# Performance work log

Measured on AMD Instinct MI355X. Metric: run time of the kernel, lower is better.

Reference implementation:

```python
import jax, jax.numpy as jnp
import numpy as np
from functools import partial

DIM = 192
HEADS = 8
DN = ('NCHW', 'OIHW', 'NCHW')


def conv1x1(x, w):
    # w: [O, I, 1, 1]
    return jax.lax.conv_general_dilated(x, w, (1, 1), 'VALID', dimension_numbers=DN)


def dwconv3x3(x, w):
    # w: [C, 1, 3, 3], depthwise
    return jax.lax.conv_general_dilated(x, w, (1, 1), 'SAME', dimension_numbers=DN,
                                        feature_group_count=x.shape[1])


def l2norm(x, eps=1e-12):
    n = jnp.sqrt(jnp.sum(x * x, axis=-1, keepdims=True))
    return x / jnp.maximum(n, eps)


def compute_attention(q, k_s, v_s, k_c, v_c, temperature, beta):
    b, c, h, w = q.shape
    hw = h * w
    r = lambda t: t.reshape(b, HEADS, c // HEADS, hw)  # b head c (h w)
    qn = l2norm(r(q))
    ks = l2norm(r(k_s))
    kc = l2norm(r(k_c))
    vs, vc = r(v_s), r(v_c)
    # channel-wise attention: [b, head, c, c]
    sa = jax.nn.softmax(jnp.einsum('bhcn,bhdn->bhcd', qn, ks) * temperature, axis=-1)
    so = jnp.einsum('bhcd,bhdn->bhcn', sa, vs)
    ca = jax.nn.softmax(-(jnp.einsum('bhcn,bhdn->bhcd', qn, kc) * temperature), axis=-1)
    co = jnp.einsum('bhcd,bhdn->bhcn', ca, vc)
    out = jax.nn.sigmoid(beta) * so + co
    return out.reshape(b, c, h, w)


def setup_inputs() -> dict:
    key = jax.random.key(0)
    ks = jax.random.split(key, 8)
    B, C, H, W = 8, DIM, 128, 128
    s = 0.02
    return {
        'x1': jax.random.normal(ks[0], (B, C, H, W), jnp.float32),
        'x2': jax.random.normal(ks[1], (B, C, H, W), jnp.float32),
        'w_qkv1': jax.random.normal(ks[2], (3 * C, C, 1, 1), jnp.float32) * s,
        'w_dw1': jax.random.normal(ks[3], (3 * C, 1, 3, 3), jnp.float32) * s,
        'w_qkv2': jax.random.normal(ks[4], (3 * C, C, 1, 1), jnp.float32) * s,
        'w_dw2': jax.random.normal(ks[5], (3 * C, 1, 3, 3), jnp.float32) * s,
        'w_proj': jax.random.normal(ks[6], (C, C, 1, 1), jnp.float32) * s,
        'temperature': jnp.ones((HEADS, 1, 1), jnp.float32),
        'beta': jnp.zeros((1,), jnp.float32),
    }


def reference(x1, x2, w_qkv1, w_dw1, w_qkv2, w_dw2, w_proj, temperature, beta):
    qkv1 = dwconv3x3(conv1x1(x1, w_qkv1), w_dw1)
    q1, k1, v1 = jnp.split(qkv1, 3, axis=1)
    qkv2 = dwconv3x3(conv1x1(x2, w_qkv2), w_dw2)
    q2, k2, v2 = jnp.split(qkv2, 3, axis=1)
    e1 = compute_attention(q1, k1, v1, k2, v2, temperature, beta)
    e2 = compute_attention(q2, k2, v2, k1, v1, temperature, beta)
    return conv1x1(e1, w_proj), conv1x1(e2, w_proj)
```

## Files before the change

kernel.cpp:

```cpp
#include <hip/hip_runtime.h>

typedef unsigned short u16;
typedef unsigned int u32;

#define NB 8
#define NCH 192
#define NC3 576
#define NHW 16384
#define NHEADS 8

typedef __attribute__((ext_vector_type(8))) short s16x8;
typedef __attribute__((ext_vector_type(4))) float f32x4;

__device__ __forceinline__ float bf2f(u32 h) {
  return __uint_as_float(h << 16);
}
__device__ __forceinline__ u16 f2bf(float f) {
  u32 u = __float_as_uint(f);
  u = (u + 0x7fffu + ((u >> 16) & 1u)) >> 16;
  return (u16)u;
}
__device__ __forceinline__ u32 pk2(u16 a, u16 b) { return (u32)a | ((u32)b << 16); }

__device__ __forceinline__ int swz(int row) { return ((row >> 1) & 7) << 4; }

__device__ __forceinline__ void gl_lds16(const void* g, void* s) {
  __builtin_amdgcn_global_load_lds((const __attribute__((address_space(1))) unsigned int*)g,
                                   (__attribute__((address_space(3))) unsigned int*)s, 16, 0, 0);
}

__global__ __launch_bounds__(256) void wcast_kernel(
    const float* __restrict__ w1, const float* __restrict__ w2,
    u16* __restrict__ o1, u16* __restrict__ o2, float* __restrict__ norms2,
    float* __restrict__ G) {
  int i = blockIdx.x * 256 + threadIdx.x;
  if (i < NC3 * NCH) {
    o1[i] = f2bf(w1[i]);
    o2[i] = f2bf(w2[i]);
  }
  if (i < 4 * NB * NCH) norms2[i] = 0.f;
  if (i < NB * NHEADS * 2304) G[i] = 0.f;
}

__device__ __forceinline__ void conv_b_load(const float* __restrict__ x, int b, int nbase,
                                            int kb, int w, int l, float2 (&val)[16]) {
  const float* xr = x + (((size_t)(b * NCH + kb + w * 16)) << 14) + nbase + l * 2;
#pragma unroll
  for (int jj = 0; jj < 16; ++jj)
    val[jj] = *(const float2*)(xr + ((size_t)jj << 14));
}

__device__ __forceinline__ void conv_b_write(char* smem, int w, int l,
                                             const float2 (&val)[16]) {
#pragma unroll
  for (int nn = 0; nn < 2; ++nn) {
    const int row = l * 2 + nn;
    u32 p[8];
#pragma unroll
    for (int q = 0; q < 8; ++q) {
      const float a = nn ? val[2 * q].y : val[2 * q].x;
      const float bb = nn ? val[2 * q + 1].y : val[2 * q + 1].x;
      p[q] = pk2(f2bf(a), f2bf(bb));
    }
    char* base = smem + 49152 + row * 128;
    *(uint4*)(base + ((w * 32 + 0) ^ swz(row))) = make_uint4(p[0], p[1], p[2], p[3]);
    *(uint4*)(base + ((w * 32 + 16) ^ swz(row))) = make_uint4(p[4], p[5], p[6], p[7]);
  }
}

__device__ __forceinline__ void conv_a_glds(char* smem, const u16* __restrict__ wbf,
                                            int obase, int kb, int w, int l, int buf) {
#pragma unroll
  for (int i = 0; i < 6; ++i) {
    const int grp = i * 4 + w;
    const int row = grp * 8 + (l >> 3);
    const int cb = ((l & 7) * 16) ^ swz(row);
    const char* src = (const char*)wbf + (size_t)(obase + row) * 384 + kb * 2 + cb;
    gl_lds16(src, smem + buf * 24576 + grp * 1024);
  }
}

__global__ __launch_bounds__(256) void conv_mfma_kernel(
    const float* __restrict__ x1, const u16* __restrict__ wbf1, u16* __restrict__ pre1,
    const float* __restrict__ x2, const u16* __restrict__ wbf2, u16* __restrict__ pre2) {
  __shared__ char smem[65536];
  const int bid = blockIdx.x;
  const int id = (bid & 7) * 768 + (bid >> 3);
  const int mod = (id >= 3072) ? 1 : 0;
  const int idm = id - mod * 3072;
  const float* x = mod ? x2 : x1;
  const u16* wbf = mod ? wbf2 : wbf1;
  u16* pre = mod ? pre2 : pre1;
  const int b = idm / 384;
  const int rr = idm % 384;
  const int nbase = (rr / 3) * 128;
  const int obase = (rr % 3) * 192;
  const int tid = threadIdx.x;
  const int w = tid >> 6, l = tid & 63;
  const int wr = w >> 1, wc = w & 1;

  f32x4 acc[6][4];
#pragma unroll
  for (int m = 0; m < 6; ++m)
#pragma unroll
    for (int nf = 0; nf < 4; ++nf) acc[m][nf] = (f32x4)0.f;

  float2 fB[16];
  conv_b_load(x, b, nbase, 0, w, l, fB);
  conv_a_glds(smem, wbf, obase, 0, w, l, 0);
  conv_b_write(smem, w, l, fB);
  __syncthreads();

  for (int t = 0; t < 3; ++t) {
    const int cur = t & 1;
    const int nxt = cur ^ 1;
    if (t < 2) {
      conv_b_load(x, b, nbase, (t + 1) * 64, w, l, fB);
      conv_a_glds(smem, wbf, obase, (t + 1) * 64, w, l, nxt);
    }
#pragma unroll
    for (int kk = 0; kk < 2; ++kk) {
      s16x8 a[6], bv[4];
      const int cbk = kk * 64 + (l >> 4) * 16;
#pragma unroll
      for (int m = 0; m < 6; ++m) {
        const int rowA = wr * 96 + m * 16 + (l & 15);
        a[m] = *(const s16x8*)(smem + cur * 24576 + rowA * 128 + (cbk ^ swz(rowA)));
      }
#pragma unroll
      for (int nf = 0; nf < 4; ++nf) {
        const int rowB = wc * 64 + nf * 16 + (l & 15);
        bv[nf] = *(const s16x8*)(smem + 49152 + rowB * 128 + (cbk ^ swz(rowB)));
      }
#pragma unroll
      for (int m = 0; m < 6; ++m)
#pragma unroll
        for (int nf = 0; nf < 4; ++nf)
          acc[m][nf] = __builtin_amdgcn_mfma_f32_16x16x32_bf16(a[m], bv[nf], acc[m][nf], 0, 0, 0);
    }
    __syncthreads();
    if (t < 2) {
      conv_b_write(smem, w, l, fB);
      __syncthreads();
    }
  }
  u16* cw = (u16*)(smem) + w * 16 * 72;
#pragma unroll
  for (int m = 0; m < 6; ++m) {
#pragma unroll
    for (int nf = 0; nf < 4; ++nf)
#pragma unroll
      for (int r = 0; r < 4; ++r)
        cw[((l >> 4) * 4 + r) * 72 + nf * 16 + (l & 15)] = f2bf(acc[m][nf][r]);
#pragma unroll
    for (int p = 0; p < 2; ++p) {
      const int chunk = p * 64 + l;
      const int row = chunk >> 3, cg = chunk & 7;
      uint4 v = *(const uint4*)(cw + row * 72 + cg * 8);
      const int o = obase + wr * 96 + m * 16 + row;
      const int n = nbase + wc * 64 + cg * 8;
      *(uint4*)(pre + (((size_t)b * NC3 + o) << 14) + n) = v;
    }
  }
}

__device__ __forceinline__ void dw_body(float* red, const u16* __restrict__ in,
                                        const float* __restrict__ wdw, u16* __restrict__ out,
                                        float* __restrict__ norms2, const int mod,
                                        const size_t t, const int tid) {
  const int l = tid & 63;
  const int xc = (int)(t & 15);
  const int yy = (int)((t >> 4) & 127);
  const int bc = (int)(t >> 11);
  const int c = bc % NC3;
  const int b = bc / NC3;
  const u16* p = in + ((size_t)bc << 14);
  const float* wc = wdw + c * 9;
  const int x0 = xc * 8;

  float a[3][10];
#pragma unroll
  for (int r = 0; r < 3; ++r) {
    const int y2 = yy + r - 1;
    if ((unsigned)y2 < 128u) {
      const u16* row = p + (y2 << 7);
      uint4 v = *(const uint4*)(row + x0);
      a[r][1] = bf2f(v.x & 0xffff); a[r][2] = bf2f(v.x >> 16);
      a[r][3] = bf2f(v.y & 0xffff); a[r][4] = bf2f(v.y >> 16);
      a[r][5] = bf2f(v.z & 0xffff); a[r][6] = bf2f(v.z >> 16);
      a[r][7] = bf2f(v.w & 0xffff); a[r][8] = bf2f(v.w >> 16);
    } else {
#pragma unroll
      for (int j = 1; j < 9; ++j) a[r][j] = 0.f;
    }
    const float lf = __shfl(a[r][8], (l - 1) & 63, 64);
    const float rt = __shfl(a[r][1], (l + 1) & 63, 64);
    a[r][0] = (xc > 0) ? lf : 0.f;
    a[r][9] = (xc < 15) ? rt : 0.f;
  }
  const float w00 = wc[0], w01 = wc[1], w02 = wc[2];
  const float w10 = wc[3], w11 = wc[4], w12 = wc[5];
  const float w20 = wc[6], w21 = wc[7], w22 = wc[8];
  u16 o[8];
  float ssq = 0.f;
#pragma unroll
  for (int j = 0; j < 8; ++j) {
    float s = a[0][j] * w00;
    s = fmaf(a[0][j + 1], w01, s);
    s = fmaf(a[0][j + 2], w02, s);
    s = fmaf(a[1][j], w10, s);
    s = fmaf(a[1][j + 1], w11, s);
    s = fmaf(a[1][j + 2], w12, s);
    s = fmaf(a[2][j], w20, s);
    s = fmaf(a[2][j + 1], w21, s);
    s = fmaf(a[2][j + 2], w22, s);
    ssq = fmaf(s, s, ssq);
    o[j] = f2bf(s);
  }
  *(uint4*)(out + (t << 3)) =
      make_uint4(pk2(o[0], o[1]), pk2(o[2], o[3]), pk2(o[4], o[5]), pk2(o[6], o[7]));

  if (c < 384) {
#pragma unroll
    for (int off = 32; off > 0; off >>= 1) ssq += __shfl_down(ssq, off, 64);
    if ((tid & 63) == 0) red[tid >> 6] = ssq;
    __syncthreads();
    if (tid == 0) {
      const int tt = (c < 192) ? mod : 2 + mod;
      atomicAdd(&norms2[(tt * NB + b) * NCH + (c % NCH)], red[0] + red[1] + red[2] + red[3]);
    }
  }
}

__global__ __launch_bounds__(256) void dwconv_kernel(
    const u16* __restrict__ in, const float* __restrict__ wdw, u16* __restrict__ out,
    float* __restrict__ norms2, const int mod) {
  __shared__ float red[4];
  dw_body(red, in, wdw, out, norms2, mod,
          (size_t)blockIdx.x * 256 + threadIdx.x, threadIdx.x);
}

__global__ __launch_bounds__(256) void dwm_kernel(
    const u16* __restrict__ pre1, const float* __restrict__ wdw1, u16* __restrict__ qkv1,
    const u16* __restrict__ pre2, const float* __restrict__ wdw2, u16* __restrict__ qkv2,
    float* __restrict__ norms2) {
  __shared__ float red[4];
  const size_t t = (size_t)blockIdx.x * 256 + threadIdx.x;
  const int bc = (int)(t >> 11);
  const int mod = (bc >= NB * NC3) ? 1 : 0;
  const size_t tm = t - ((size_t)mod * NB * NC3 << 11);
  if (mod)
    dw_body(red, pre2, wdw2, qkv2, norms2, 1, tm, threadIdx.x);
  else
    dw_body(red, pre1, wdw1, qkv1, norms2, 0, tm, threadIdx.x);
}

__global__ __launch_bounds__(256) void gram_mfma_kernel(
    const u16* __restrict__ qkv1, const u16* __restrict__ qkv2, float* __restrict__ G) {
  const int nc = blockIdx.x, h = blockIdx.y, b = blockIdx.z;
  const int tid = threadIdx.x;
  const int w = tid >> 6, l = tid & 63;

  const u16* qp[3];
  const u16* kp[3];
#pragma unroll
  for (int m = 0; m < 3; ++m) {
    const int rq = m * 16 + (l & 15);
    const int cc = h * 24 + (rq < 24 ? rq : rq - 24);
    const u16* basep = (rq < 24) ? qkv1 : qkv2;
    qp[m] = basep + (((size_t)b * NC3 + cc) << 14);
    kp[m] = basep + (((size_t)b * NC3 + 192 + cc) << 14);
  }
  const int kbase = nc * 1024 + w * 256 + (l >> 4) * 8;

  f32x4 acc[3][3];
#pragma unroll
  for (int m = 0; m < 3; ++m)
#pragma unroll
    for (int nf = 0; nf < 3; ++nf) acc[m][nf] = (f32x4)0.f;

  for (int t = 0; t < 8; ++t) {
    const int ko = kbase + t * 32;
    s16x8 a[3], bv[3];
#pragma unroll
    for (int m = 0; m < 3; ++m) {
      a[m] = *(const s16x8*)(qp[m] + ko);
      bv[m] = *(const s16x8*)(kp[m] + ko);
    }
#pragma unroll
    for (int m = 0; m < 3; ++m)
#pragma unroll
      for (int nf = 0; nf < 3; ++nf)
        acc[m][nf] = __builtin_amdgcn_mfma_f32_16x16x32_bf16(a[m], bv[nf], acc[m][nf], 0, 0, 0);
  }

  __shared__ float red[4][48][48];
#pragma unroll
  for (int m = 0; m < 3; ++m)
#pragma unroll
    for (int nf = 0; nf < 3; ++nf)
#pragma unroll
      for (int r = 0; r < 4; ++r)
        red[w][m * 16 + (l >> 4) * 4 + r][nf * 16 + (l & 15)] = acc[m][nf][r];
  __syncthreads();
  float* dst = G + ((size_t)b * 8 + h) * 2304;
  for (int e = tid; e < 2304; e += 256) {
    const int rr = e / 48, cc = e % 48;
    atomicAdd(&dst[e], red[0][rr][cc] + red[1][rr][cc] + red[2][rr][cc] + red[3][rr][cc]);
  }
}

__global__ __launch_bounds__(256) void softmax_wcat_kernel(
    const float* __restrict__ G, const float* __restrict__ norms2,
    const float* __restrict__ temperature, const float* __restrict__ beta,
    const float* __restrict__ wproj, u16* __restrict__ Wcat) {
  const int bh = blockIdx.x;
  const int b = bh >> 3, h = bh & 7;
  __shared__ float sm[4][24][24];
  __shared__ float nrm[4][24];
  const int tid = threadIdx.x;
  if (tid < 96) {
    int t = tid / 24, ci = tid % 24;
    nrm[t][ci] = fmaxf(sqrtf(norms2[(t * NB + b) * NCH + h * 24 + ci]), 1e-12f);
  }
  __syncthreads();
  const float T = temperature[h];
  const float sigB = 1.f / (1.f + expf(-beta[0]));
  if (tid < 96) {
    const int m = tid / 24, r = tid % 24;
    const float* Gb = G + (size_t)bh * 2304;
    const int gr = (m >= 2) ? 24 + r : r;
    const int gc0 = (m == 1 || m == 2) ? 24 : 0;
    const float* qn = (m >= 2) ? nrm[1] : nrm[0];
    const float* kn = (m == 1 || m == 2) ? nrm[3] : nrm[2];
    const float sign = (m == 0 || m == 2) ? 1.f : -1.f;
    const float qs = sign * T / qn[r];
    float L[24], mx = -1e30f;
#pragma unroll
    for (int cc = 0; cc < 24; ++cc) {
      L[cc] = Gb[gr * 48 + gc0 + cc] * qs / kn[cc];
      mx = fmaxf(mx, L[cc]);
    }
    float ssum = 0.f;
#pragma unroll
    for (int cc = 0; cc < 24; ++cc) {
      L[cc] = expf(L[cc] - mx);
      ssum += L[cc];
    }
    const float inv = 1.f / ssum;
#pragma unroll
    for (int cc = 0; cc < 24; ++cc) sm[m][r][cc] = L[cc] * inv;
  }
  __syncthreads();
  for (int e = tid; e < 384 * 48; e += 256) {
    const int o = e / 48, dc = e % 48;
    const int part = dc / 24, d = dc % 24;
    const int oc = (o < 192) ? o : o - 192;
    int m;
    float scale;
    if (o < 192) { m = part ? 1 : 0; scale = part ? 1.f : sigB; }
    else         { m = part ? 2 : 3; scale = part ? sigB : 1.f; }
    float s = 0.f;
#pragma unroll
    for (int ci = 0; ci < 24; ++ci) s += wproj[oc * 192 + h * 24 + ci] * sm[m][ci][d];
    Wcat[((size_t)b * 384 + o) * 384 + part * 192 + h * 24 + d] = f2bf(s * scale);
  }
}

__device__ __forceinline__ void fin_b_load(const u16* __restrict__ qkv1,
                                           const u16* __restrict__ qkv2,
                                           int b, int nbase, int kb, int w, int l,
                                           u32 (&val)[16]) {
  const u16* vbase = (kb < 192) ? qkv1 + (((size_t)b * NC3 + 384 + kb) << 14)
                                : qkv2 + (((size_t)b * NC3 + 384 + kb - 192) << 14);
  const u16* p0 = vbase + (((size_t)(w * 16)) << 14) + nbase + l * 2;
#pragma unroll
  for (int jj = 0; jj < 16; ++jj)
    val[jj] = *(const u32*)(p0 + ((size_t)jj << 14));
}

__device__ __forceinline__ void fin_b_write(char* smem, int w, int l,
                                            const u32 (&val)[16]) {
#pragma unroll
  for (int nn = 0; nn < 2; ++nn) {
    const int row = l * 2 + nn;
    u32 p[8];
#pragma unroll
    for (int q = 0; q < 8; ++q) {
      const u32 a = (val[2 * q] >> (nn * 16)) & 0xffffu;
      const u32 bb = (val[2 * q + 1] >> (nn * 16)) & 0xffffu;
      p[q] = a | (bb << 16);
    }
    char* base = smem + 32768 + row * 128;
    *(uint4*)(base + ((w * 32 + 0) ^ swz(row))) = make_uint4(p[0], p[1], p[2], p[3]);
    *(uint4*)(base + ((w * 32 + 16) ^ swz(row))) = make_uint4(p[4], p[5], p[6], p[7]);
  }
}

__device__ __forceinline__ void fin_a_glds(char* smem, const u16* __restrict__ Wcat,
                                           int b, int obase, int kb, int w, int l, int buf) {
#pragma unroll
  for (int i = 0; i < 4; ++i) {
    const int grp = i * 4 + w;
    const int row = grp * 8 + (l >> 3);
    const int cb = ((l & 7) * 16) ^ swz(row);
    const char* src = (const char*)Wcat + ((size_t)b * 384 + obase + row) * 768 + kb * 2 + cb;
    gl_lds16(src, smem + buf * 16384 + grp * 1024);
  }
}

__global__ __launch_bounds__(256) void final_mfma_kernel(
    const u16* __restrict__ qkv1, const u16* __restrict__ qkv2,
    const u16* __restrict__ Wcat, float* __restrict__ out) {
  __shared__ char smem[49152];
  const int bid = blockIdx.x;
  const int id = (bid & 7) * 384 + (bid >> 3);
  const int b = id / 384;
  const int rr2 = id % 384;
  const int nbase = (rr2 / 3) * 128;
  const int obase = (rr2 % 3) * 128;
  const int tid = threadIdx.x;
  const int w = tid >> 6, l = tid & 63;
  const int wr = w >> 1, wc = w & 1;

  f32x4 acc[4][4];
#pragma unroll
  for (int m = 0; m < 4; ++m)
#pragma unroll
    for (int nf = 0; nf < 4; ++nf) acc[m][nf] = (f32x4)0.f;

  u32 fV[16];
  fin_b_load(qkv1, qkv2, b, nbase, 0, w, l, fV);
  fin_a_glds(smem, Wcat, b, obase, 0, w, l, 0);
  fin_b_write(smem, w, l, fV);
  __syncthreads();

  for (int t = 0; t < 6; ++t) {
    const int cur = t & 1;
    const int nxt = cur ^ 1;
    if (t < 5) {
      fin_b_load(qkv1, qkv2, b, nbase, (t + 1) * 64, w, l, fV);
      fin_a_glds(smem, Wcat, b, obase, (t + 1) * 64, w, l, nxt);
    }
#pragma unroll
    for (int kk = 0; kk < 2; ++kk) {
      s16x8 a[4], bv[4];
      const int cbk = kk * 64 + (l >> 4) * 16;
#pragma unroll
      for (int m = 0; m < 4; ++m) {
        const int rowA = wr * 64 + m * 16 + (l & 15);
        a[m] = *(const s16x8*)(smem + cur * 16384 + rowA * 128 + (cbk ^ swz(rowA)));
      }
#pragma unroll
      for (int nf = 0; nf < 4; ++nf) {
        const int rowB = wc * 64 + nf * 16 + (l & 15);
        bv[nf] = *(const s16x8*)(smem + 32768 + rowB * 128 + (cbk ^ swz(rowB)));
      }
#pragma unroll
      for (int m = 0; m < 4; ++m)
#pragma unroll
        for (int nf = 0; nf < 4; ++nf)
          acc[m][nf] = __builtin_amdgcn_mfma_f32_16x16x32_bf16(a[m], bv[nf], acc[m][nf], 0, 0, 0);
    }
    __syncthreads();
    if (t < 5) {
      fin_b_write(smem, w, l, fV);
      __syncthreads();
    }
  }
  float* cw = (float*)(smem + w * 4352);
#pragma unroll
  for (int m = 0; m < 4; ++m) {
#pragma unroll
    for (int nf = 0; nf < 4; ++nf)
#pragma unroll
      for (int r = 0; r < 4; ++r)
        cw[((l >> 4) * 4 + r) * 68 + nf * 16 + (l & 15)] = acc[m][nf][r];
#pragma unroll
    for (int p = 0; p < 4; ++p) {
      const int chunk = p * 64 + l;
      const int row = chunk >> 4, cg = chunk & 15;
      f32x4 v = *(const f32x4*)(cw + row * 68 + cg * 4);
      const int o = obase + wr * 64 + m * 16 + row;
      const int n = nbase + wc * 64 + cg * 4;
      float* dst = (o < 192) ? out + (((size_t)b * NCH + o) << 14) + n
                             : out + 25165824 + (((size_t)b * NCH + o - 192) << 14) + n;
      __builtin_nontemporal_store(v, (f32x4*)dst);
    }
  }
}

extern "C" void kernel_launch(void* const* d_in, const int* in_sizes, int n_in,
                              void* d_out, int out_size, void* d_ws, size_t ws_size,
                              hipStream_t stream) {
  (void)in_sizes; (void)n_in; (void)out_size;
  const float* x1 = (const float*)d_in[0];
  const float* x2 = (const float*)d_in[1];
  const float* w_qkv1 = (const float*)d_in[2];
  const float* w_dw1 = (const float*)d_in[3];
  const float* w_qkv2 = (const float*)d_in[4];
  const float* w_dw2 = (const float*)d_in[5];
  const float* w_proj = (const float*)d_in[6];
  const float* temperature = (const float*)d_in[7];
  const float* beta = (const float*)d_in[8];
  float* out = (float*)d_out;

  char* wsb = (char*)d_ws;
  const size_t BUF = 150994944;
  const bool big = ws_size >= 607395840;

  u16* pre1 = (u16*)(wsb);
  u16* qkv1 = (u16*)(wsb + BUF);
  u16* pre2 = (u16*)(wsb + 2 * BUF);
  u16* qkv2 = big ? (u16*)(wsb + 3 * BUF) : pre1;
  char* tail = big ? (wsb + 4 * BUF) : (wsb + 3 * BUF);
  u16* wbf1 = (u16*)(tail);
  u16* wbf2 = (u16*)(tail + 221184);
  float* norms2 = (float*)(tail + 442368);
  float* G = (float*)(tail + 466944);
  u16* WcatBf = (u16*)(tail + 1056768);

  const int dwblocks = (int)(((size_t)NB * NC3 * NHW) / (256 * 8));

  wcast_kernel<<<576, 256, 0, stream>>>(w_qkv1, w_qkv2, wbf1, wbf2, norms2, G);
  conv_mfma_kernel<<<6144, 256, 0, stream>>>(x1, wbf1, pre1, x2, wbf2, pre2);
  if (big) {
    dwm_kernel<<<2 * dwblocks, 256, 0, stream>>>(pre1, w_dw1, qkv1, pre2, w_dw2, qkv2, norms2);
  } else {
    dwconv_kernel<<<dwblocks, 256, 0, stream>>>(pre1, w_dw1, qkv1, norms2, 0);
    dwconv_kernel<<<dwblocks, 256, 0, stream>>>(pre2, w_dw2, qkv2, norms2, 1);
  }
  gram_mfma_kernel<<<dim3(16, NHEADS, NB), 256, 0, stream>>>(qkv1, qkv2, G);
  softmax_wcat_kernel<<<NB * NHEADS, 256, 0, stream>>>(G, norms2, temperature, beta, w_proj, WcatBf);
  final_mfma_kernel<<<3072, 256, 0, stream>>>(qkv1, qkv2, WcatBf, out);
}
```

Baseline: 477.8 us.

## Single-buffer conv LDS for occupancy and compute two output rows per dwconv thread

```diff
diff --git a/kernel.cpp b/kernel.cpp
--- a/kernel.cpp
+++ b/kernel.cpp
@@ -62,28 +62,28 @@
       const float bb = nn ? val[2 * q + 1].y : val[2 * q + 1].x;
       p[q] = pk2(f2bf(a), f2bf(bb));
     }
-    char* base = smem + 49152 + row * 128;
+    char* base = smem + 24576 + row * 128;
     *(uint4*)(base + ((w * 32 + 0) ^ swz(row))) = make_uint4(p[0], p[1], p[2], p[3]);
     *(uint4*)(base + ((w * 32 + 16) ^ swz(row))) = make_uint4(p[4], p[5], p[6], p[7]);
   }
 }
 
 __device__ __forceinline__ void conv_a_glds(char* smem, const u16* __restrict__ wbf,
-                                            int obase, int kb, int w, int l, int buf) {
+                                            int obase, int kb, int w, int l) {
 #pragma unroll
   for (int i = 0; i < 6; ++i) {
     const int grp = i * 4 + w;
     const int row = grp * 8 + (l >> 3);
     const int cb = ((l & 7) * 16) ^ swz(row);
     const char* src = (const char*)wbf + (size_t)(obase + row) * 384 + kb * 2 + cb;
-    gl_lds16(src, smem + buf * 24576 + grp * 1024);
+    gl_lds16(src, smem + grp * 1024);
   }
 }
 
 __global__ __launch_bounds__(256) void conv_mfma_kernel(
     const float* __restrict__ x1, const u16* __restrict__ wbf1, u16* __restrict__ pre1,
     const float* __restrict__ x2, const u16* __restrict__ wbf2, u16* __restrict__ pre2) {
-  __shared__ char smem[65536];
+  __shared__ char smem[40960];
   const int bid = blockIdx.x;
   const int id = (bid & 7) * 768 + (bid >> 3);
   const int mod = (id >= 3072) ? 1 : 0;
@@ -107,17 +107,12 @@
 
   float2 fB[16];
   conv_b_load(x, b, nbase, 0, w, l, fB);
-  conv_a_glds(smem, wbf, obase, 0, w, l, 0);
-  conv_b_write(smem, w, l, fB);
-  __syncthreads();
 
   for (int t = 0; t < 3; ++t) {
-    const int cur = t & 1;
-    const int nxt = cur ^ 1;
-    if (t < 2) {
-      conv_b_load(x, b, nbase, (t + 1) * 64, w, l, fB);
-      conv_a_glds(smem, wbf, obase, (t + 1) * 64, w, l, nxt);
-    }
+    conv_a_glds(smem, wbf, obase, t * 64, w, l);
+    conv_b_write(smem, w, l, fB);
+    if (t < 2) conv_b_load(x, b, nbase, (t + 1) * 64, w, l, fB);
+    __syncthreads();
 #pragma unroll
     for (int kk = 0; kk < 2; ++kk) {
       s16x8 a[6], bv[4];
@@ -125,12 +120,12 @@
 #pragma unroll
       for (int m = 0; m < 6; ++m) {
         const int rowA = wr * 96 + m * 16 + (l & 15);
-        a[m] = *(const s16x8*)(smem + cur * 24576 + rowA * 128 + (cbk ^ swz(rowA)));
+        a[m] = *(const s16x8*)(smem + rowA * 128 + (cbk ^ swz(rowA)));
       }
 #pragma unroll
       for (int nf = 0; nf < 4; ++nf) {
         const int rowB = wc * 64 + nf * 16 + (l & 15);
-        bv[nf] = *(const s16x8*)(smem + 49152 + rowB * 128 + (cbk ^ swz(rowB)));
+        bv[nf] = *(const s16x8*)(smem + 24576 + rowB * 128 + (cbk ^ swz(rowB)));
       }
 #pragma unroll
       for (int m = 0; m < 6; ++m)
@@ -139,10 +134,6 @@
           acc[m][nf] = __builtin_amdgcn_mfma_f32_16x16x32_bf16(a[m], bv[nf], acc[m][nf], 0, 0, 0);
     }
     __syncthreads();
-    if (t < 2) {
-      conv_b_write(smem, w, l, fB);
-      __syncthreads();
-    }
   }
   u16* cw = (u16*)(smem) + w * 16 * 72;
 #pragma unroll
@@ -170,18 +161,19 @@
                                         const size_t t, const int tid) {
   const int l = tid & 63;
   const int xc = (int)(t & 15);
-  const int yy = (int)((t >> 4) & 127);
-  const int bc = (int)(t >> 11);
+  const int yp = (int)((t >> 4) & 63);
+  const int bc = (int)(t >> 10);
   const int c = bc % NC3;
   const int b = bc / NC3;
   const u16* p = in + ((size_t)bc << 14);
   const float* wc = wdw + c * 9;
   const int x0 = xc * 8;
-
-  float a[3][10];
-#pragma unroll
-  for (int r = 0; r < 3; ++r) {
-    const int y2 = yy + r - 1;
+  const int y0 = yp * 2;
+
+  float a[4][10];
+#pragma unroll
+  for (int r = 0; r < 4; ++r) {
+    const int y2 = y0 + r - 1;
     if ((unsigned)y2 < 128u) {
       const u16* row = p + (y2 << 7);
       uint4 v = *(const uint4*)(row + x0);
@@ -201,24 +193,27 @@
   const float w00 = wc[0], w01 = wc[1], w02 = wc[2];
   const float w10 = wc[3], w11 = wc[4], w12 = wc[5];
   const float w20 = wc[6], w21 = wc[7], w22 = wc[8];
-  u16 o[8];
   float ssq = 0.f;
 #pragma unroll
-  for (int j = 0; j < 8; ++j) {
-    float s = a[0][j] * w00;
-    s = fmaf(a[0][j + 1], w01, s);
-    s = fmaf(a[0][j + 2], w02, s);
-    s = fmaf(a[1][j], w10, s);
-    s = fmaf(a[1][j + 1], w11, s);
-    s = fmaf(a[1][j + 2], w12, s);
-    s = fmaf(a[2][j], w20, s);
-    s = fmaf(a[2][j + 1], w21, s);
-    s = fmaf(a[2][j + 2], w22, s);
-    ssq = fmaf(s, s, ssq);
-    o[j] = f2bf(s);
-  }
-  *(uint4*)(out + (t << 3)) =
-      make_uint4(pk2(o[0], o[1]), pk2(o[2], o[3]), pk2(o[4], o[5]), pk2(o[6], o[7]));
+  for (int nn = 0; nn < 2; ++nn) {
+    u16 o[8];
+#pragma unroll
+    for (int j = 0; j < 8; ++j) {
+      float s = a[nn][j] * w00;
+      s = fmaf(a[nn][j + 1], w01, s);
+      s = fmaf(a[nn][j + 2], w02, s);
+      s = fmaf(a[nn + 1][j], w10, s);
+      s = fmaf(a[nn + 1][j + 1], w11, s);
+      s = fmaf(a[nn + 1][j + 2], w12, s);
+      s = fmaf(a[nn + 2][j], w20, s);
+      s = fmaf(a[nn + 2][j + 1], w21, s);
+      s = fmaf(a[nn + 2][j + 2], w22, s);
+      ssq = fmaf(s, s, ssq);
+      o[j] = f2bf(s);
+    }
+    *(uint4*)(out + ((size_t)bc << 14) + ((y0 + nn) << 7) + x0) =
+        make_uint4(pk2(o[0], o[1]), pk2(o[2], o[3]), pk2(o[4], o[5]), pk2(o[6], o[7]));
+  }
 
   if (c < 384) {
 #pragma unroll
@@ -246,9 +241,9 @@
     float* __restrict__ norms2) {
   __shared__ float red[4];
   const size_t t = (size_t)blockIdx.x * 256 + threadIdx.x;
-  const int bc = (int)(t >> 11);
+  const int bc = (int)(t >> 10);
   const int mod = (bc >= NB * NC3) ? 1 : 0;
-  const size_t tm = t - ((size_t)mod * NB * NC3 << 11);
+  const size_t tm = t - ((size_t)mod * NB * NC3 << 10);
   if (mod)
     dw_body(red, pre2, wdw2, qkv2, norms2, 1, tm, threadIdx.x);
   else
@@ -520,7 +515,7 @@
   float* G = (float*)(tail + 466944);
   u16* WcatBf = (u16*)(tail + 1056768);
 
-  const int dwblocks = (int)(((size_t)NB * NC3 * NHW) / (256 * 8));
+  const int dwblocks = (int)(((size_t)NB * NC3 * NHW) / (256 * 16));
 
   wcast_kernel<<<576, 256, 0, stream>>>(w_qkv1, w_qkv2, wbf1, wbf2, norms2, G);
   conv_mfma_kernel<<<6144, 256, 0, stream>>>(x1, wbf1, pre1, x2, wbf2, pre2);
```

After: 450.8 us (median of 2 runs). 5.6% less time.
